# Kernel optimization log

Hardware: AMD Instinct MI355X
Metric: run time of the kernel (lower is better)

## Reference

```python
import jax, jax.numpy as jnp
import numpy as np

STRIDE = 2  # ksize = [1, STRIDE, 1, 1]: unpool along height only
B, H, W, C = 8, 512, 256, 64


def setup_inputs() -> dict:
    key = jax.random.key(0)
    k1, k2 = jax.random.split(key)
    inputs = jax.random.normal(k1, (B, H, W, C), dtype=jnp.float32)
    # TF argmax-style flat indices into the per-batch output grid [2H, W, C]
    mask = jax.random.randint(k2, (B, H, W, C), 0, STRIDE * H * W * C, dtype=jnp.int64)
    return {"inputs": inputs, "mask": mask}


def reference(inputs, mask):
    b_, h, w, c = inputs.shape
    out_h = h * STRIDE  # output_shape = (B, stride*H, W, C)
    # Decode flat per-batch indices exactly as the TF layer does
    y = mask // (w * c)
    x = (mask % (w * c)) // c
    b = jnp.arange(b_, dtype=jnp.int64)[:, None, None, None]  # batch_range
    f = jnp.arange(c, dtype=jnp.int64)                        # feature_range
    # tf.scatter_nd sums duplicate indices; .at[].add matches that semantics
    out = jnp.zeros((b_, out_h, w, c), dtype=inputs.dtype)
    out = out.at[b, y, x, f].add(inputs)
    return out
```

## Files before the change

kernel.cpp:

```cpp
#include <hip/hip_runtime.h>


typedef unsigned int u32;
typedef unsigned short u16;
typedef unsigned long long u64;

typedef int   iv4 __attribute__((ext_vector_type(4)));
typedef float fv4 __attribute__((ext_vector_type(4)));

constexpr long long N_IN = 1LL << 26;
constexpr int SBS   = 8192;
constexpr int NSB   = (int)(N_IN / SBS);
constexpr int NBKT  = 1024;
constexpr int NWIN  = 8192;
constexpr int RSH   = 14;
constexpr int RSLOTS = 1 << RSH;
constexpr int SB_PER_B = 1024;

constexpr size_t OFF_RECA = 0;
constexpr size_t OFF_DIR  = (size_t)N_IN * 8;
constexpr size_t OFF_DIRT = OFF_DIR + (size_t)NSB * NBKT * 2;
constexpr size_t WS_FUSED = OFF_DIRT + (size_t)NWIN * SB_PER_B * 2;

__global__ __launch_bounds__(512) void passA(const float* __restrict__ in,
                                             const int* __restrict__ mask,
                                             u64* __restrict__ recA,
                                             u16* __restrict__ dir)
{
    __shared__ u32 cur[NBKT];
    __shared__ u32 wsum[8];
    __shared__ u64 sRec[SBS];
    const int tid = threadIdx.x;
    const int sb  = blockIdx.x;
    const int e0  = sb * SBS + tid * 16;

    const iv4* m4 = (const iv4*)mask + (e0 >> 2);
    const fv4* v4 = (const fv4*)in + (e0 >> 2);
    iv4 m0 = __builtin_nontemporal_load(m4 + 0);
    iv4 m1 = __builtin_nontemporal_load(m4 + 1);
    iv4 m2 = __builtin_nontemporal_load(m4 + 2);
    iv4 m3 = __builtin_nontemporal_load(m4 + 3);
    fv4 va = __builtin_nontemporal_load(v4 + 0);
    fv4 vb = __builtin_nontemporal_load(v4 + 1);
    fv4 vc = __builtin_nontemporal_load(v4 + 2);
    fv4 vd = __builtin_nontemporal_load(v4 + 3);
    const u32 bbits = ((u32)(e0 >> 23)) << 24;
    const u32 c0 = (u32)(e0 & 63);

    u32 tg[16]; float vv[16];
    tg[ 0] = bbits + (((u32)m0.x) & ~63u) + c0 +  0; vv[ 0] = va.x;
    tg[ 1] = bbits + (((u32)m0.y) & ~63u) + c0 +  1; vv[ 1] = va.y;
    tg[ 2] = bbits + (((u32)m0.z) & ~63u) + c0 +  2; vv[ 2] = va.z;
    tg[ 3] = bbits + (((u32)m0.w) & ~63u) + c0 +  3; vv[ 3] = va.w;
    tg[ 4] = bbits + (((u32)m1.x) & ~63u) + c0 +  4; vv[ 4] = vb.x;
    tg[ 5] = bbits + (((u32)m1.y) & ~63u) + c0 +  5; vv[ 5] = vb.y;
    tg[ 6] = bbits + (((u32)m1.z) & ~63u) + c0 +  6; vv[ 6] = vb.z;
    tg[ 7] = bbits + (((u32)m1.w) & ~63u) + c0 +  7; vv[ 7] = vb.w;
    tg[ 8] = bbits + (((u32)m2.x) & ~63u) + c0 +  8; vv[ 8] = vc.x;
    tg[ 9] = bbits + (((u32)m2.y) & ~63u) + c0 +  9; vv[ 9] = vc.y;
    tg[10] = bbits + (((u32)m2.z) & ~63u) + c0 + 10; vv[10] = vc.z;
    tg[11] = bbits + (((u32)m2.w) & ~63u) + c0 + 11; vv[11] = vc.w;
    tg[12] = bbits + (((u32)m3.x) & ~63u) + c0 + 12; vv[12] = vd.x;
    tg[13] = bbits + (((u32)m3.y) & ~63u) + c0 + 13; vv[13] = vd.y;
    tg[14] = bbits + (((u32)m3.z) & ~63u) + c0 + 14; vv[14] = vd.z;
    tg[15] = bbits + (((u32)m3.w) & ~63u) + c0 + 15; vv[15] = vd.w;

    cur[2 * tid] = 0;
    cur[2 * tid + 1] = 0;
    __syncthreads();
#pragma unroll
    for (int j = 0; j < 16; ++j) atomicAdd(&cur[(tg[j] >> RSH) & (NBKT - 1)], 1u);
    __syncthreads();

    {
        const int lane = tid & 63;
        const int wid  = tid >> 6;
        u32 a = cur[2 * tid];
        u32 b = cur[2 * tid + 1];
        u32 sum = a + b;
        u32 s = sum;
#pragma unroll
        for (int d = 1; d < 64; d <<= 1) {
            u32 n = __shfl_up(s, (unsigned)d, 64);
            if (lane >= d) s += n;
        }
        if (lane == 63) wsum[wid] = s;
        u32 exw = s - sum;
        __syncthreads();
        if (tid == 0) {
            u32 run = 0;
#pragma unroll
            for (int w = 0; w < 8; ++w) { u32 t2 = wsum[w]; wsum[w] = run; run += t2; }
        }
        __syncthreads();
        u32 start = wsum[wid] + exw;
        dir[(size_t)sb * NBKT + 2 * tid]     = (u16)start;
        dir[(size_t)sb * NBKT + 2 * tid + 1] = (u16)(start + a);
        cur[2 * tid]     = start;
        cur[2 * tid + 1] = start + a;
    }
    __syncthreads();

#pragma unroll
    for (int j = 0; j < 16; ++j) {
        u32 p = atomicAdd(&cur[(tg[j] >> RSH) & (NBKT - 1)], 1u);
        sRec[p] = ((u64)(tg[j] & (RSLOTS - 1)) << 32) | (u64)__float_as_uint(vv[j]);
    }
    __syncthreads();
#pragma unroll
    for (int k = 0; k < 16; ++k) {
        int i = tid + k * 512;
        recA[(size_t)sb * SBS + i] = sRec[i];
    }
}

__global__ __launch_bounds__(256) void tposeD(const u16* __restrict__ dir,
                                              u16* __restrict__ dirT)
{
    __shared__ u16 t[64][65];
    const int tx = threadIdx.x;
    const int ty = threadIdx.y;
    const int bb = blockIdx.z;
    const int sb0 = blockIdx.x * 64;
    const int lb0 = blockIdx.y * 64;
#pragma unroll
    for (int k = 0; k < 16; ++k) {
        int row = k * 4 + ty;
        t[row][tx] = dir[((size_t)(bb * SB_PER_B + sb0 + row)) * NBKT + lb0 + tx];
    }
    __syncthreads();
#pragma unroll
    for (int k = 0; k < 16; ++k) {
        int row = k * 4 + ty;
        dirT[((size_t)(bb * NBKT + lb0 + row)) * SB_PER_B + sb0 + tx] = t[tx][row];
    }
}

__global__ __launch_bounds__(1024, 8) void passC(const u64* __restrict__ recA,
                                                 const u16* __restrict__ dirT,
                                                 float* __restrict__ out)
{
    __shared__ float acc[RSLOTS];
    __shared__ u32 cSrc[SB_PER_B];
    __shared__ u16 cLen[SB_PER_B];
    const int tid = threadIdx.x;
    const int bid = blockIdx.x;
    const int w   = ((bid & 7) << 10) | (bid >> 3);
    const int bb  = w >> 10;
    const int lb  = w & (NBKT - 1);

    {
        u32 st = dirT[(size_t)w * SB_PER_B + tid];
        u32 en = (lb == NBKT - 1) ? (u32)SBS : (u32)dirT[(size_t)(w + 1) * SB_PER_B + tid];
        cSrc[tid] = (u32)(bb * SB_PER_B + tid) * (u32)SBS + st;
        cLen[tid] = (u16)(en - st);
    }
    {
        fv4 z = {0.f, 0.f, 0.f, 0.f};
        fv4* av = (fv4*)acc;
#pragma unroll
        for (int i = tid; i < RSLOTS / 4; i += 1024) av[i] = z;
    }
    __syncthreads();

    const int g  = tid >> 4;
    const int gl = tid & 15;
#pragma unroll
    for (int r = 0; r < 2; ++r) {
        u32 src[8]; int len[8]; u64 rec[8];
#pragma unroll
        for (int j = 0; j < 8; ++j) {
            int s = g + (r * 8 + j) * 64;
            src[j] = cSrc[s];
            len[j] = (int)cLen[s];
        }
#pragma unroll
        for (int j = 0; j < 8; ++j) rec[j] = recA[src[j] + gl];
#pragma unroll
        for (int j = 0; j < 8; ++j) {
            if (gl < len[j])
                atomicAdd(&acc[(u32)(rec[j] >> 32)], __uint_as_float((u32)rec[j]));
        }
#pragma unroll
        for (int j = 0; j < 8; ++j) {
            for (int off = gl + 16; off < len[j]; off += 16) {
                u64 rc = recA[src[j] + off];
                atomicAdd(&acc[(u32)(rc >> 32)], __uint_as_float((u32)rc));
            }
        }
    }
    __syncthreads();

    fv4* o4 = (fv4*)out + ((size_t)w << (RSH - 2));
    const fv4* a4 = (const fv4*)acc;
#pragma unroll
    for (int i = tid; i < RSLOTS / 4; i += 1024)
        __builtin_nontemporal_store(a4[i], o4 + i);
}

__global__ __launch_bounds__(256) void unmaxpool_scatter(
    const float* __restrict__ in, const int* __restrict__ mask,
    float* __restrict__ out)
{
    const long long n4 = N_IN / 4;
    long long gidx = (long long)blockIdx.x * blockDim.x + threadIdx.x;
    const long long stride = (long long)gridDim.x * blockDim.x;
    for (; gidx < n4; gidx += stride) {
        float4 v = reinterpret_cast<const float4*>(in)[gidx];
        int4 m = reinterpret_cast<const int4*>(mask)[gidx];
        long long i0 = gidx * 4;
        u32 ob = ((u32)(i0 >> 23)) << 24;
        u32 c0 = (u32)(i0 & 63);
        atomicAdd(&out[ob + (u32)(m.x & ~63) + c0 + 0], v.x);
        atomicAdd(&out[ob + (u32)(m.y & ~63) + c0 + 1], v.y);
        atomicAdd(&out[ob + (u32)(m.z & ~63) + c0 + 2], v.z);
        atomicAdd(&out[ob + (u32)(m.w & ~63) + c0 + 3], v.w);
    }
}

extern "C" void kernel_launch(void* const* d_in, const int* in_sizes, int n_in,
                              void* d_out, int out_size, void* d_ws, size_t ws_size,
                              hipStream_t stream) {
    const float* in = (const float*)d_in[0];
    const int* mask = (const int*)d_in[1];
    float* out = (float*)d_out;
    char* ws = (char*)d_ws;

    if (d_ws != nullptr && ws_size >= WS_FUSED) {
        u64* recA = (u64*)(ws + OFF_RECA);
        u16* dir  = (u16*)(ws + OFF_DIR);
        u16* dirT = (u16*)(ws + OFF_DIRT);
        passA<<<NSB, 512, 0, stream>>>(in, mask, recA, dir);
        tposeD<<<dim3(16, 16, 8), dim3(64, 4), 0, stream>>>(dir, dirT);
        passC<<<NWIN, 1024, 0, stream>>>(recA, dirT, out);
    } else {
        (void)hipMemsetAsync(out, 0, (size_t)out_size * sizeof(float), stream);
        unmaxpool_scatter<<<2048, 256, 0, stream>>>(in, mask, out);
    }
}
```

Baseline: 632.5 us.

## Stage passC record reads through async global-to-LDS loads with software pipeline

The scatter-accumulate kernel now fetches the first 16 records of every chunk with direct global-to-LDS loads. Each wave keeps four staging buffers in flight and waits on vmcnt counters, so atomic accumulation into shared memory overlaps with the next fetches. Records beyond the first 16 of a chunk are handled by one lane per chunk in a serial loop. The cost is an extra 64KB LDS staging buffer and a dropped min-blocks hint, which likely cuts resident blocks per CU. Long chunks also get only one lane each, which can serialise the tail work.

```diff
diff --git a/kernel.cpp b/kernel.cpp
--- a/kernel.cpp
+++ b/kernel.cpp
@@ -136,18 +136,21 @@
     }
 }
 
-__global__ __launch_bounds__(1024, 8) void passC(const u64* __restrict__ recA,
-                                                 const u16* __restrict__ dirT,
-                                                 float* __restrict__ out)
+__global__ __launch_bounds__(1024) void passC(const u64* __restrict__ recA,
+                                              const u16* __restrict__ dirT,
+                                              float* __restrict__ out)
 {
     __shared__ float acc[RSLOTS];
+    __shared__ u64 stage[16][4][128];
     __shared__ u32 cSrc[SB_PER_B];
     __shared__ u16 cLen[SB_PER_B];
-    const int tid = threadIdx.x;
-    const int bid = blockIdx.x;
-    const int w   = ((bid & 7) << 10) | (bid >> 3);
-    const int bb  = w >> 10;
-    const int lb  = w & (NBKT - 1);
+    const int tid  = threadIdx.x;
+    const int bid  = blockIdx.x;
+    const int w    = ((bid & 7) << 10) | (bid >> 3);
+    const int bb   = w >> 10;
+    const int lb   = w & (NBKT - 1);
+    const int wv   = tid >> 6;
+    const int lane = tid & 63;
 
     {
         u32 st = dirT[(size_t)w * SB_PER_B + tid];
@@ -163,30 +166,54 @@
     }
     __syncthreads();
 
-    const int g  = tid >> 4;
-    const int gl = tid & 15;
-#pragma unroll
-    for (int r = 0; r < 2; ++r) {
-        u32 src[8]; int len[8]; u64 rec[8];
-#pragma unroll
-        for (int j = 0; j < 8; ++j) {
-            int s = g + (r * 8 + j) * 64;
-            src[j] = cSrc[s];
-            len[j] = (int)cLen[s];
-        }
-#pragma unroll
-        for (int j = 0; j < 8; ++j) rec[j] = recA[src[j] + gl];
-#pragma unroll
-        for (int j = 0; j < 8; ++j) {
-            if (gl < len[j])
-                atomicAdd(&acc[(u32)(rec[j] >> 32)], __uint_as_float((u32)rec[j]));
-        }
-#pragma unroll
-        for (int j = 0; j < 8; ++j) {
-            for (int off = gl + 16; off < len[j]; off += 16) {
-                u64 rc = recA[src[j] + off];
-                atomicAdd(&acc[(u32)(rc >> 32)], __uint_as_float((u32)rc));
-            }
+    const int cw = wv * 64;
+    const u64* ga[8];
+#pragma unroll
+    for (int g2 = 0; g2 < 8; ++g2)
+        ga[g2] = recA + (size_t)cSrc[cw + g2 * 8 + (lane >> 3)] + (size_t)((lane & 7) << 1);
+
+#define ISSUE(G, SLOT)                                                         \
+    __builtin_amdgcn_global_load_lds(                                          \
+        (const __attribute__((address_space(1))) void*)ga[G],                  \
+        (__attribute__((address_space(3))) void*)&stage[wv][SLOT][0], 16, 0, 0)
+
+#define WAITV(N)                                                               \
+    asm volatile("s_waitcnt vmcnt(" #N ")" ::: "memory");                      \
+    __builtin_amdgcn_sched_barrier(0)
+
+#define PROC(G)                                                                \
+    {                                                                          \
+        u64 r0 = stage[wv][(G) & 3][lane];                                     \
+        u64 r1 = stage[wv][(G) & 3][lane + 64];                                \
+        const int cA = cw + (G) * 8 + (lane >> 4);                             \
+        const int cB = cA + 4;                                                 \
+        const int ri = lane & 15;                                              \
+        if (ri < (int)cLen[cA])                                                \
+            atomicAdd(&acc[(u32)(r0 >> 32)], __uint_as_float((u32)r0));        \
+        if (ri < (int)cLen[cB])                                                \
+            atomicAdd(&acc[(u32)(r1 >> 32)], __uint_as_float((u32)r1));        \
+    }
+
+    ISSUE(0, 0); ISSUE(1, 1); ISSUE(2, 2); ISSUE(3, 3);
+    WAITV(3); PROC(0); ISSUE(4, 0);
+    WAITV(3); PROC(1); ISSUE(5, 1);
+    WAITV(3); PROC(2); ISSUE(6, 2);
+    WAITV(3); PROC(3); ISSUE(7, 3);
+    WAITV(3); PROC(4);
+    WAITV(2); PROC(5);
+    WAITV(1); PROC(6);
+    WAITV(0); PROC(7);
+
+#undef ISSUE
+#undef WAITV
+#undef PROC
+
+    {
+        const int c   = cw + lane;
+        const int len = (int)cLen[c];
+        for (int off = 16; off < len; ++off) {
+            u64 rc = recA[(size_t)cSrc[c] + off];
+            atomicAdd(&acc[(u32)(rc >> 32)], __uint_as_float((u32)rc));
         }
     }
     __syncthreads();
```

After: 744.8 us. 17.8% more time.
